# Kernel tuning notes

Hardware: AMD Instinct MI355X
Metric: run time of the kernel (lower is better)

The kernel has to match this reference:

```python
import jax, jax.numpy as jnp
import numpy as np

B, L, D, H = 1, 4096, 1024, 16
HD = D // H  # head dim = 64
WINDOW = 15


def _rope(t, cos, sin):
    # t: [B,H,L,HD]; cos/sin: [1,1,L,HD//2]
    tr = t.reshape(*t.shape[:-1], HD // 2, 2)
    a, b = tr[..., 0], tr[..., 1]
    out_r = a * cos - b * sin
    out_i = a * sin + b * cos
    return jnp.stack([out_r, out_i], axis=-1).reshape(t.shape)


def _longformer_mask(L, window):
    i = jnp.arange(L)[:, None]
    j = jnp.arange(L)[None, :]
    causal = j <= i
    win = jnp.abs(i - j) <= window // 2
    glob = (j == 0) | (i == 0)
    return (causal & win) | glob  # [L,L] bool


def setup_inputs() -> dict:
    key = jax.random.key(0)
    kx, kq, kk, kv, ko = jax.random.split(key, 5)
    x = jax.random.normal(kx, (B, L, D), dtype=jnp.float32)
    scale = 0.02
    Wq = jax.random.normal(kq, (D, D), dtype=jnp.float32) * scale
    Wk = jax.random.normal(kk, (D, D), dtype=jnp.float32) * scale
    Wv = jax.random.normal(kv, (D, D), dtype=jnp.float32) * scale
    Wo = jax.random.normal(ko, (D, D), dtype=jnp.float32) * scale
    # real RoPE frequencies (complex freqs_cis split into cos/sin)
    inv_freq = 1.0 / (10000.0 ** (np.arange(0, HD, 2, dtype=np.float32) / HD))
    pos = np.arange(L, dtype=np.float32)
    ang = pos[:, None] * inv_freq[None, :]  # [L, HD//2]
    freqs_cos = jnp.asarray(np.cos(ang))[None]  # [1,L,HD//2]
    freqs_sin = jnp.asarray(np.sin(ang))[None]
    return {"x": x, "Wq": Wq, "Wk": Wk, "Wv": Wv, "Wo": Wo,
            "freqs_cos": freqs_cos, "freqs_sin": freqs_sin}


def reference(x, Wq, Wk, Wv, Wo, freqs_cos, freqs_sin):
    b, l, _ = x.shape
    # projections (nn.Linear: y = x @ W^T)
    Q = (x @ Wq.T).reshape(b, l, H, HD).transpose(0, 2, 1, 3)  # [B,H,L,HD]
    K = (x @ Wk.T).reshape(b, l, H, HD).transpose(0, 2, 1, 3)
    V = (x @ Wv.T).reshape(b, l, H, HD).transpose(0, 2, 1, 3)
    cos = freqs_cos[:, None, :l]  # [1,1,L,HD//2] (torch unsqueeze(1))
    sin = freqs_sin[:, None, :l]
    Q = _rope(Q, cos, sin)
    K = _rope(K, cos, sin)
    mask = _longformer_mask(l, WINDOW)  # [L,L]
    scores = jnp.einsum('bhqd,bhkd->bhqk', Q, K) / jnp.sqrt(jnp.float32(HD))
    scores = jnp.where(mask[None, None], scores, jnp.finfo(scores.dtype).min)
    attn = jax.nn.softmax(scores, axis=-1)
    out = jnp.einsum('bhqk,bhkd->bhqd', attn, V)  # [B,H,L,HD]
    out = out.transpose(0, 2, 1, 3).reshape(b, l, D)
    return out @ Wo.T
```

## Files before the change

kernel.cpp:

```cpp
#include <hip/hip_runtime.h>
#include <stdint.h>

#define SL 4096
#define DM 1024
#define NH 16
#define HDIM 64

typedef short short8 __attribute__((ext_vector_type(8)));
typedef float f32x4 __attribute__((ext_vector_type(4)));

__device__ __forceinline__ unsigned short f2bf(float f) {
  unsigned int u = __float_as_uint(f);
  u += 0x7FFF + ((u >> 16) & 1);
  return (unsigned short)(u >> 16);
}
__device__ __forceinline__ float bf2f(unsigned short u) {
  return __uint_as_float((unsigned int)u << 16);
}
__device__ __forceinline__ float bflo(unsigned int u) { return __uint_as_float(u << 16); }
__device__ __forceinline__ float bfhi(unsigned int u) { return __uint_as_float(u & 0xffff0000u); }

__device__ __forceinline__ void gload_lds16(const void* g, void* l) {
  __builtin_amdgcn_global_load_lds((const __attribute__((address_space(1))) void*)g,
                                   (__attribute__((address_space(3))) void*)l, 16, 0, 0);
}

__global__ void cast_all(const float* __restrict__ x,
                         const float* __restrict__ Wq, const float* __restrict__ Wk,
                         const float* __restrict__ Wv, const float* __restrict__ Wo,
                         unsigned short* __restrict__ xb,
                         unsigned short* __restrict__ w3b, unsigned short* __restrict__ wob) {
  int i = blockIdx.x * blockDim.x + threadIdx.x;
  const float* src;
  unsigned short* dst;
  int off;
  if (i < (1 << 20)) {
    src = x; dst = xb; off = i;
  } else {
    int wsel = i - (1 << 20);
    int seg = wsel >> 18;
    off = wsel & 262143;
    src = (seg == 0) ? Wq : (seg == 1) ? Wk : (seg == 2) ? Wv : Wo;
    dst = (seg < 3) ? (w3b + (size_t)seg * DM * DM) : wob;
  }
  float4 v = ((const float4*)src)[off];
  ushort4 o = make_ushort4(f2bf(v.x), f2bf(v.y), f2bf(v.z), f2bf(v.w));
  ((ushort4*)dst)[off] = o;
}

template <int BM, int BN, bool BF16OUT, bool ROPE>
__global__ void gemm_bt(const unsigned short* __restrict__ A,
                        const unsigned short* __restrict__ B,
                        void* __restrict__ Cv,
                        int M, int N, int K, int ldc,
                        const float* __restrict__ fc, const float* __restrict__ fs) {
  constexpr int WM = BM / 64, WN = BN / 64, W = WM * WN;
  constexpr int ACW = BM / 16 / W;
  constexpr int BCW = BN / 16 / W;
  __shared__ __align__(16) unsigned short As[2][BM * 32];
  __shared__ __align__(16) unsigned short Bs[2][BN * 32];
  const int tid  = threadIdx.x;
  const int w    = tid >> 6;
  const int lane = tid & 63;
  const int wr = w / WN, wc = w % WN;

  const int gx = gridDim.x;
  const int total = gx * gridDim.y;
  const int lin = blockIdx.y * gx + blockIdx.x;
  const int swz = (lin & 7) * (total >> 3) + (lin >> 3);
  const int brow = (swz / gx) * BM;
  const int bcol = (swz % gx) * BN;

  const int l4 = lane >> 2;
  const int lkS = (((lane & 3) ^ ((lane >> 3) & 3))) * 8;
  const int lrow = lane & 15;
  const int sw8 = (((lane >> 4) ^ ((lane >> 1) & 3))) * 8;

  const unsigned short* Ag[ACW];
  const unsigned short* Bg[BCW];
#pragma unroll
  for (int c = 0; c < ACW; ++c)
    Ag[c] = A + (size_t)(brow + (w * ACW + c) * 16 + l4) * K + lkS;
#pragma unroll
  for (int c = 0; c < BCW; ++c)
    Bg[c] = B + (size_t)(bcol + (w * BCW + c) * 16 + l4) * K + lkS;

  f32x4 acc[4][4] = {};
  const int NT = K >> 5;

  auto STAGE = [&](int t, int b) {
    const int k0 = t << 5;
#pragma unroll
    for (int c = 0; c < ACW; ++c) gload_lds16(Ag[c] + k0, &As[b][(w * ACW + c) * 512]);
#pragma unroll
    for (int c = 0; c < BCW; ++c) gload_lds16(Bg[c] + k0, &Bs[b][(w * BCW + c) * 512]);
  };
  auto COMPUTE = [&](int cur) {
    short8 af[4], bf[4];
#pragma unroll
    for (int m = 0; m < 4; ++m)
      af[m] = *(const short8*)&As[cur][(wr * 64 + m * 16 + lrow) * 32 + sw8];
#pragma unroll
    for (int n = 0; n < 4; ++n)
      bf[n] = *(const short8*)&Bs[cur][(wc * 64 + n * 16 + lrow) * 32 + sw8];
#pragma unroll
    for (int m = 0; m < 4; ++m)
#pragma unroll
      for (int n = 0; n < 4; ++n)
        acc[m][n] = __builtin_amdgcn_mfma_f32_16x16x32_bf16(af[m], bf[n], acc[m][n], 0, 0, 0);
  };

  STAGE(0, 0);
  for (int t = 0; t < NT; ++t) {
    const int cur = t & 1;
    __syncthreads();
    if (t + 1 < NT) STAGE(t + 1, cur ^ 1);
    COMPUTE(cur);
  }

  const int er = (lane >> 4) * 4;
  const int ec = lane & 15;

  if constexpr (ROPE) {
    if (bcol + wc * 64 < 2048) {
#pragma unroll
      for (int n = 0; n < 4; ++n) {
        const int p = ((n * 16 + ec) & 63) >> 1;
#pragma unroll
        for (int m = 0; m < 4; ++m) {
#pragma unroll
          for (int r = 0; r < 4; ++r) {
            const int row = brow + wr * 64 + m * 16 + er + r;
            float v = acc[m][n][r];
            float pv = __shfl_xor(v, 1);
            float cs = fc[row * 32 + p], sn = fs[row * 32 + p];
            acc[m][n][r] = (lane & 1) ? (pv * sn + v * cs) : (v * cs - pv * sn);
          }
        }
      }
    }
  }

#pragma unroll
  for (int m = 0; m < 4; ++m)
#pragma unroll
    for (int n = 0; n < 4; ++n) {
      const size_t roff = (size_t)(brow + wr * 64 + m * 16 + er) * ldc + (bcol + wc * 64 + n * 16 + ec);
      if constexpr (BF16OUT) {
        unsigned short* cp = (unsigned short*)Cv + roff;
#pragma unroll
        for (int r = 0; r < 4; ++r) cp[(size_t)r * ldc] = f2bf(acc[m][n][r]);
      } else {
        float* cp = (float*)Cv + roff;
#pragma unroll
        for (int r = 0; r < 4; ++r) cp[(size_t)r * ldc] = acc[m][n][r];
      }
    }
}

__global__ __launch_bounds__(256)
void attn_fused(const unsigned short* __restrict__ qkv, unsigned short* __restrict__ atb,
                float* __restrict__ prt) {
  const int wid = threadIdx.x >> 6;
  const int lane = threadIdx.x & 63;
  if (blockIdx.x >= 1024) {
    const int u = (blockIdx.x - 1024) * 4 + wid;
    const int p = u & 127, h = u >> 7;
    const float q = bf2f(qkv[h * 64 + lane]);
    float m = -1e30f, s = 0.f, o = 0.f;
    const int j0 = p * 32;
    for (int jj = 0; jj < 32; ++jj) {
      const int j = j0 + jj;
      float kv = bf2f(qkv[(size_t)j * 3072 + 1024 + h * 64 + lane]);
      float pr = q * kv;
#pragma unroll
      for (int off = 32; off; off >>= 1) pr += __shfl_xor(pr, off);
      pr *= 0.125f;
      float mn = fmaxf(m, pr);
      float c = __expf(m - mn);
      float e = __expf(pr - mn);
      float v = bf2f(qkv[(size_t)j * 3072 + 2048 + h * 64 + lane]);
      s = s * c + e;
      o = o * c + e * v;
      m = mn;
    }
    float* dst = prt + ((size_t)h * 128 + p) * 72;
    if (lane == 0) { dst[0] = m; dst[1] = s; }
    dst[2 + lane] = o;
    return;
  }

  const int i = blockIdx.x * 4 + wid + 1;
  if (i >= SL) return;
  const unsigned short* rowQ = qkv + (size_t)i * 3072 + lane * 16;

  float q[16];
  {
    uint4 a = *(const uint4*)rowQ;
    uint4 b = *(const uint4*)(rowQ + 8);
    unsigned int uu[8] = {a.x, a.y, a.z, a.w, b.x, b.y, b.z, b.w};
#pragma unroll
    for (int c = 0; c < 8; ++c) { q[2 * c] = bflo(uu[c]); q[2 * c + 1] = bfhi(uu[c]); }
  }

  float sc[9];
#pragma unroll
  for (int t = 0; t < 9; ++t) {
    int j = (t == 0) ? 0 : (i - 8 + t);
    bool valid = (t == 0) || (j >= 1);
    int jc = valid ? j : 0;
    const unsigned short* pk = qkv + (size_t)jc * 3072 + 1024 + lane * 16;
    uint4 a = *(const uint4*)pk;
    uint4 b = *(const uint4*)(pk + 8);
    unsigned int uu[8] = {a.x, a.y, a.z, a.w, b.x, b.y, b.z, b.w};
    float pr = 0.f;
#pragma unroll
    for (int c = 0; c < 8; ++c) pr += bflo(uu[c]) * q[2 * c] + bfhi(uu[c]) * q[2 * c + 1];
    pr += __shfl_xor(pr, 1);
    pr += __shfl_xor(pr, 2);
    sc[t] = valid ? pr * 0.125f : -1e30f;
  }

  float mx = sc[0];
#pragma unroll
  for (int t = 1; t < 9; ++t) mx = fmaxf(mx, sc[t]);
  float s = 0.f;
#pragma unroll
  for (int t = 0; t < 9; ++t) { float e = __expf(sc[t] - mx); sc[t] = e; s += e; }
  const float inv = 1.0f / s;

  float o[16] = {};
#pragma unroll
  for (int t = 0; t < 9; ++t) {
    int j = (t == 0) ? 0 : (i - 8 + t);
    bool valid = (t == 0) || (j >= 1);
    int jc = valid ? j : 0;
    const unsigned short* pv = qkv + (size_t)jc * 3072 + 2048 + lane * 16;
    uint4 a = *(const uint4*)pv;
    uint4 b = *(const uint4*)(pv + 8);
    unsigned int uu[8] = {a.x, a.y, a.z, a.w, b.x, b.y, b.z, b.w};
#pragma unroll
    for (int c = 0; c < 8; ++c) {
      o[2 * c]     += sc[t] * bflo(uu[c]);
      o[2 * c + 1] += sc[t] * bfhi(uu[c]);
    }
  }

  unsigned int wv[8];
#pragma unroll
  for (int c = 0; c < 8; ++c)
    wv[c] = (unsigned int)f2bf(o[2 * c] * inv) | ((unsigned int)f2bf(o[2 * c + 1] * inv) << 16);
  unsigned short* po = atb + (size_t)i * 1024 + lane * 16;
  uint4 s0; s0.x = wv[0]; s0.y = wv[1]; s0.z = wv[2]; s0.w = wv[3];
  uint4 s1; s1.x = wv[4]; s1.y = wv[5]; s1.z = wv[6]; s1.w = wv[7];
  *(uint4*)po = s0;
  *(uint4*)(po + 8) = s1;
}

__global__ __launch_bounds__(64)
void attn_row0_combine(const float* __restrict__ prt, unsigned short* __restrict__ atb) {
  const int h = blockIdx.x;
  const int lane = threadIdx.x;
  const float* base = prt + (size_t)h * 128 * 72;
  __shared__ float cbuf[128];
  float m0 = base[lane * 72];
  float m1 = base[(lane + 64) * 72];
  float M = fmaxf(m0, m1);
#pragma unroll
  for (int off = 32; off; off >>= 1) M = fmaxf(M, __shfl_xor(M, off));
  float c0 = __expf(m0 - M), c1 = __expf(m1 - M);
  float ls = base[lane * 72 + 1] * c0 + base[(lane + 64) * 72 + 1] * c1;
#pragma unroll
  for (int off = 32; off; off >>= 1) ls += __shfl_xor(ls, off);
  cbuf[lane] = c0;
  cbuf[lane + 64] = c1;
  __syncthreads();
  float o = 0.f;
#pragma unroll 8
  for (int p = 0; p < 128; ++p) o += cbuf[p] * base[p * 72 + 2 + lane];
  atb[h * 64 + lane] = f2bf(o / ls);
}

extern "C" void kernel_launch(void* const* d_in, const int* in_sizes, int n_in,
                              void* d_out, int out_size, void* d_ws, size_t ws_size,
                              hipStream_t stream) {
  const float* x  = (const float*)d_in[0];
  const float* Wq = (const float*)d_in[1];
  const float* Wk = (const float*)d_in[2];
  const float* Wv = (const float*)d_in[3];
  const float* Wo = (const float*)d_in[4];
  const float* fc = (const float*)d_in[5];
  const float* fs = (const float*)d_in[6];
  float* out = (float*)d_out;

  char* ws = (char*)d_ws;
  unsigned short* xb   = (unsigned short*)(ws);
  unsigned short* w3b  = (unsigned short*)(ws + ((size_t)8 << 20));
  unsigned short* wob  = (unsigned short*)(ws + ((size_t)14 << 20));
  unsigned short* qkvb = (unsigned short*)(ws + ((size_t)16 << 20));
  unsigned short* atb  = (unsigned short*)(ws + ((size_t)40 << 20));
  float*          prt  = (float*)(ws + ((size_t)48 << 20));

  cast_all<<<(2 * (1 << 20)) / 256, 256, 0, stream>>>(x, Wq, Wk, Wv, Wo, xb, w3b, wob);

  dim3 g1(3072 / 128, SL / 256);
  gemm_bt<256, 128, true, true><<<g1, 512, 0, stream>>>(xb, w3b, (void*)qkvb, SL, 3072, DM, 3072, fc, fs);

  attn_fused<<<1536, 256, 0, stream>>>(qkvb, atb, prt);
  attn_row0_combine<<<NH, 64, 0, stream>>>(prt, atb);

  dim3 g2(DM / 128, SL / 128);
  gemm_bt<128, 128, false, false><<<g2, 256, 0, stream>>>(atb, wob, (void*)out, SL, DM, DM, DM, nullptr, nullptr);
}
```

Measured before the change: 102.4 us.

## Shrink GEMM tiles for QKV projection and split-K output projection with reduce

The QKV projection GEMM moves from 256x128 tiles with 512 threads to 64x128 tiles with 128 threads, which gives many more blocks across the CUs. The output projection is split along K into two halves via gridDim.z; each half writes an fp32 partial to workspace and a separate reduce kernel sums the two into the output. This targets low occupancy and wave quantization on a 256-CU device. In exchange it costs an extra kernel launch and extra fp32 traffic for the partials, and smaller tiles reuse data less.

```diff
diff --git a/kernel.cpp b/kernel.cpp
--- a/kernel.cpp
+++ b/kernel.cpp
@@ -52,7 +52,7 @@
 __global__ void gemm_bt(const unsigned short* __restrict__ A,
                         const unsigned short* __restrict__ B,
                         void* __restrict__ Cv,
-                        int M, int N, int K, int ldc,
+                        int K, int lda, int ldc, size_t czstride,
                         const float* __restrict__ fc, const float* __restrict__ fs) {
   constexpr int WM = BM / 64, WN = BN / 64, W = WM * WN;
   constexpr int ACW = BM / 16 / W;
@@ -64,6 +64,10 @@
   const int lane = tid & 63;
   const int wr = w / WN, wc = w % WN;
 
+  const int kz = blockIdx.z;
+  A += (size_t)kz * K;
+  B += (size_t)kz * K;
+
   const int gx = gridDim.x;
   const int total = gx * gridDim.y;
   const int lin = blockIdx.y * gx + blockIdx.x;
@@ -80,10 +84,10 @@
   const unsigned short* Bg[BCW];
 #pragma unroll
   for (int c = 0; c < ACW; ++c)
-    Ag[c] = A + (size_t)(brow + (w * ACW + c) * 16 + l4) * K + lkS;
+    Ag[c] = A + (size_t)(brow + (w * ACW + c) * 16 + l4) * lda + lkS;
 #pragma unroll
   for (int c = 0; c < BCW; ++c)
-    Bg[c] = B + (size_t)(bcol + (w * BCW + c) * 16 + l4) * K + lkS;
+    Bg[c] = B + (size_t)(bcol + (w * BCW + c) * 16 + l4) * lda + lkS;
 
   f32x4 acc[4][4] = {};
   const int NT = K >> 5;
@@ -151,11 +155,19 @@
 #pragma unroll
         for (int r = 0; r < 4; ++r) cp[(size_t)r * ldc] = f2bf(acc[m][n][r]);
       } else {
-        float* cp = (float*)Cv + roff;
+        float* cp = (float*)Cv + kz * czstride + roff;
 #pragma unroll
         for (int r = 0; r < 4; ++r) cp[(size_t)r * ldc] = acc[m][n][r];
       }
     }
+}
+
+__global__ void reduce2(const float4* __restrict__ p0, const float4* __restrict__ p1,
+                        float4* __restrict__ out, int n4) {
+  for (int i = blockIdx.x * blockDim.x + threadIdx.x; i < n4; i += gridDim.x * blockDim.x) {
+    float4 a = p0[i], b = p1[i];
+    out[i] = make_float4(a.x + b.x, a.y + b.y, a.z + b.z, a.w + b.w);
+  }
 }
 
 __global__ __launch_bounds__(256)
@@ -300,15 +312,27 @@
   unsigned short* qkvb = (unsigned short*)(ws + ((size_t)16 << 20));
   unsigned short* atb  = (unsigned short*)(ws + ((size_t)40 << 20));
   float*          prt  = (float*)(ws + ((size_t)48 << 20));
+  float*          gp   = (float*)(ws + ((size_t)50 << 20));
 
   cast_all<<<(2 * (1 << 20)) / 256, 256, 0, stream>>>(x, Wq, Wk, Wv, Wo, xb, w3b, wob);
 
-  dim3 g1(3072 / 128, SL / 256);
-  gemm_bt<256, 128, true, true><<<g1, 512, 0, stream>>>(xb, w3b, (void*)qkvb, SL, 3072, DM, 3072, fc, fs);
+  dim3 g1(3072 / 128, SL / 64, 1);
+  gemm_bt<64, 128, true, true><<<g1, 128, 0, stream>>>(
+      xb, w3b, (void*)qkvb, DM, DM, 3072, 0, fc, fs);
 
   attn_fused<<<1536, 256, 0, stream>>>(qkvb, atb, prt);
   attn_row0_combine<<<NH, 64, 0, stream>>>(prt, atb);
 
-  dim3 g2(DM / 128, SL / 128);
-  gemm_bt<128, 128, false, false><<<g2, 256, 0, stream>>>(atb, wob, (void*)out, SL, DM, DM, DM, nullptr, nullptr);
-}
+  if (ws_size >= ((size_t)82 << 20)) {
+    dim3 g2(DM / 128, SL / 64, 2);
+    gemm_bt<64, 128, false, false><<<g2, 128, 0, stream>>>(
+        atb, wob, (void*)gp, DM / 2, DM, DM, (size_t)SL * DM, nullptr, nullptr);
+    const int n4 = SL * DM / 4;
+    reduce2<<<2048, 256, 0, stream>>>((const float4*)gp, (const float4*)(gp + (size_t)SL * DM),
+                                      (float4*)out, n4);
+  } else {
+    dim3 g2(DM / 128, SL / 128, 1);
+    gemm_bt<128, 128, false, false><<<g2, 256, 0, stream>>>(
+        atb, wob, (void*)out, DM, DM, DM, 0, nullptr, nullptr);
+  }
+}
```

After: 116.0 us. +13.3%, slower.
